# Kernel optimization log

Measured on AMD Instinct MI355X. Metric: run time of the kernel, lower is better.

## Reference

```python
import jax, jax.numpy as jnp
import numpy as np

NEG_SLOPE = 0.2
N, E, NNZ, IN, H, C = 100000, 50000, 800000, 128, 8, 16


def setup_inputs() -> dict:
    key = jax.random.key(0)
    ks = jax.random.split(key, 8)
    X = jax.random.normal(ks[0], (N, IN), jnp.float32)
    W_typed = jax.random.normal(ks[1], (4, IN, H * C), jnp.float32) * (1.0 / np.sqrt(IN))
    att_e = jax.random.normal(ks[2], (4, H, C), jnp.float32) * 0.1
    att_v = jax.random.normal(ks[3], (4, H, C), jnp.float32) * 0.1
    vertex = jax.random.randint(ks[4], (NNZ,), 0, N, jnp.int32)
    edges = jax.random.randint(ks[5], (NNZ,), 0, E, jnp.int32)
    vtype = jax.random.randint(ks[6], (N,), 0, 4, jnp.int32)
    etype = jax.random.randint(ks[7], (E,), 0, 4, jnp.int32)
    return {"X": X, "W_typed": W_typed, "att_e": att_e, "att_v": att_v,
            "vertex": vertex, "edges": edges, "vtype": vtype, "etype": etype}


def _segment_softmax(logits, seg, num):
    # numerically-stable softmax over segments (PyG-style, eps in denominator)
    m = jax.ops.segment_max(logits, seg, num_segments=num)
    ex = jnp.exp(logits - m[seg])
    s = jax.ops.segment_sum(ex, seg, num_segments=num)
    return ex / (s[seg] + 1e-16)


def reference(X, W_typed, att_e, att_v, vertex, edges, vtype, etype):
    # typed linear: project with all 4 type weights, select per node type
    Xall = jnp.einsum('ni,tio->tno', X, W_typed)        # [4, N, H*C]
    X0 = Xall[vtype, jnp.arange(N)]                     # [N, H*C]
    Xn = X0.reshape(N, H, C)
    Xve = Xn[vertex]                                    # [NNZ, H, C] gather vertex->incidence
    # vertex->edge attention, typed by edge type of each incidence
    beta = jnp.sum(Xve * att_e[etype[edges]], axis=-1)  # [NNZ, H]
    beta = jax.nn.leaky_relu(beta, NEG_SLOPE)
    beta = _segment_softmax(beta, edges, E)
    Xe = jax.nn.relu(jax.ops.segment_sum(Xve * beta[..., None], edges, num_segments=E))  # [E, H, C]
    Xe = Xe[edges]                                      # [NNZ, H, C] gather edge->incidence
    # edge->vertex attention, typed by node type of each incidence's vertex
    alpha = jnp.sum(Xe * att_v[vtype[vertex]], axis=-1)  # [NNZ, H]
    alpha = jax.nn.leaky_relu(alpha, NEG_SLOPE)
    alpha = _segment_softmax(alpha, vertex, N)
    Xv = jax.ops.segment_sum(Xe * alpha[..., None], vertex, num_segments=N)  # [N, H, C]
    return Xv.reshape(N, H * C)
```

## Files before the change

kernel.cpp:

```cpp
#include <hip/hip_runtime.h>

typedef __attribute__((ext_vector_type(8))) short bf16x8;
typedef __attribute__((ext_vector_type(4))) float f32x4;

#define NEG_SLOPE 0.2f

__device__ __forceinline__ unsigned short f2bf(float f){
  unsigned u = __float_as_uint(f);
  u = (u + 0x7fffu + ((u >> 16) & 1u)) >> 16;
  return (unsigned short)u;
}
__device__ __forceinline__ float bflo(unsigned u){ return __uint_as_float(u << 16); }
__device__ __forceinline__ float bfhi(unsigned u){ return __uint_as_float(u & 0xffff0000u); }
__device__ __forceinline__ float lrelu(float x){ return x > 0.f ? x : NEG_SLOPE * x; }

__global__ __launch_bounds__(256) void k_prep(
    const int* __restrict__ vtype, int N, int* __restrict__ tcnt, int nbHN,
    const float* __restrict__ W, short* __restrict__ Bfrag){
  __shared__ int lcnt[4];
  int b = (int)blockIdx.x;
  if (b < nbHN){
    if (threadIdx.x < 4) lcnt[threadIdx.x] = 0;
    __syncthreads();
    int i = b * 256 + threadIdx.x;
    if (i < N) atomicAdd(&lcnt[vtype[i]], 1);
    __syncthreads();
    if (threadIdx.x < 4 && lcnt[threadIdx.x] > 0)
      atomicAdd(tcnt + threadIdx.x, lcnt[threadIdx.x]);
    return;
  }
  b -= nbHN;
  int u = b * 256 + threadIdx.x;
  int j = u & 7, lane = (u >> 3) & 63, ct = (u >> 9) & 31, ks = u >> 14;
  int k = ks * 32 + ((lane >> 4) << 3) + j;
  int col = (ct << 4) + (lane & 15);
  int t = col >> 7, o = col & 127;
  Bfrag[u] = (short)f2bf(W[(t * 128 + k) * 128 + o]);
}

__global__ void k_pbase(const int* __restrict__ tcnt, int* __restrict__ pbase){
  if (threadIdx.x == 0 && blockIdx.x == 0){
    int pb = 0;
    for (int t = 0; t < 4; ++t){
      pbase[t] = pb;
      pb += ((tcnt[t] + 63) >> 6) << 6;
    }
    pbase[4] = pb;
  }
}

__global__ __launch_bounds__(256) void k_nodeplace(
    const int* __restrict__ vtype, int N, const int* __restrict__ pbase,
    int* __restrict__ tcur, int* __restrict__ nsorted){
  __shared__ int lcnt[4];
  __shared__ int gbase[4];
  int t = threadIdx.x;
  if (t < 4) lcnt[t] = 0;
  __syncthreads();
  int i = (int)blockIdx.x * 256 + t;
  int tt = 0, rank = 0;
  bool valid = i < N;
  if (valid){ tt = vtype[i]; rank = atomicAdd(&lcnt[tt], 1); }
  __syncthreads();
  if (t < 4 && lcnt[t] > 0) gbase[t] = atomicAdd(tcur + t, lcnt[t]);
  __syncthreads();
  if (valid) nsorted[pbase[tt] + gbase[tt] + rank] = i;
}

__global__ __launch_bounds__(256, 3) void k_gemm_hist(const float* __restrict__ X,
    const short* __restrict__ Bfrag, const int* __restrict__ nsorted,
    const int* __restrict__ pbase, unsigned short* __restrict__ X0,
    const int* __restrict__ edges, const int* __restrict__ vertex, int NNZ,
    int* __restrict__ cnt, int E,
    int* __restrict__ rank_e, int* __restrict__ rank_v, int nbHist){
  __shared__ short shB[8 * 4 * 64 * 8];
  const int tid = threadIdx.x;
  const int q = (int)blockIdx.x / 3, r = (int)blockIdx.x % 3;

  if (r != 0){
    int hb = 2 * q + (r - 1);
    if (hb < nbHist){
      int i = hb * 256 + tid;
      if (i < NNZ){
        rank_e[i] = atomicAdd(cnt + edges[i], 1);
        rank_v[i] = atomicAdd(cnt + E + vertex[i], 1);
      }
    }
    return;
  }

  const int rowIdx = q * 64;
  const int t = (rowIdx >= pbase[1]) + (rowIdx >= pbase[2]) + (rowIdx >= pbase[3]);

  const bf16x8* Bv = (const bf16x8*)Bfrag;
  bf16x8* shBv = (bf16x8*)shB;
  #pragma unroll
  for (int v = 0; v < 8; ++v){
    int item = v * 256 + tid;
    int slab = item >> 6, ln = item & 63;
    int ks = slab >> 3, ctl = slab & 7;
    shBv[item] = Bv[((ks * 32 + 8 * t + ctl) * 64) + ln];
  }

  const int w = tid >> 6, lane = tid & 63;
  const int m = lane & 15, qq = lane >> 4;
  const int node = nsorted[rowIdx + w * 16 + m];

  bf16x8 afrag[4];
  #pragma unroll
  for (int ks = 0; ks < 4; ++ks){
    bf16x8 f;
    if (node >= 0){
      const float4* src = (const float4*)(X + (size_t)node * 128 + ks * 32 + qq * 8);
      float4 a = src[0], b = src[1];
      f[0]=(short)f2bf(a.x); f[1]=(short)f2bf(a.y); f[2]=(short)f2bf(a.z); f[3]=(short)f2bf(a.w);
      f[4]=(short)f2bf(b.x); f[5]=(short)f2bf(b.y); f[6]=(short)f2bf(b.z); f[7]=(short)f2bf(b.w);
    } else {
      #pragma unroll
      for (int z = 0; z < 8; ++z) f[z] = 0;
    }
    afrag[ks] = f;
  }

  f32x4 acc[8];
  #pragma unroll
  for (int ct = 0; ct < 8; ++ct){
    acc[ct][0]=0.f; acc[ct][1]=0.f; acc[ct][2]=0.f; acc[ct][3]=0.f;
  }

  __syncthreads();
  #pragma unroll
  for (int ctl = 0; ctl < 8; ++ctl){
    #pragma unroll
    for (int ks = 0; ks < 4; ++ks){
      bf16x8 bf = shBv[(ks * 8 + ctl) * 64 + lane];
      acc[ctl] = __builtin_amdgcn_mfma_f32_16x16x32_bf16(afrag[ks], bf, acc[ctl], 0, 0, 0);
    }
  }

  const int col0 = lane & 15;
  #pragma unroll
  for (int rr = 0; rr < 4; ++rr){
    int row = nsorted[rowIdx + w * 16 + qq * 4 + rr];
    if (row < 0) continue;
    #pragma unroll
    for (int ctl = 0; ctl < 8; ++ctl)
      X0[(size_t)row * 128 + ctl * 16 + col0] = f2bf(acc[ctl][rr]);
  }
}

__global__ __launch_bounds__(256) void k_scanA(const int* __restrict__ cnt, int S,
                                               int* __restrict__ bsum){
  __shared__ int sh[256];
  int base = blockIdx.x * 1024 + threadIdx.x * 4;
  int s = 0;
  #pragma unroll
  for (int k = 0; k < 4; ++k){ int idx = base + k; if (idx < S) s += cnt[idx]; }
  sh[threadIdx.x] = s; __syncthreads();
  for (int off = 128; off > 0; off >>= 1){
    if (threadIdx.x < off) sh[threadIdx.x] += sh[threadIdx.x + off];
    __syncthreads();
  }
  if (threadIdx.x == 0) bsum[blockIdx.x] = sh[0];
}

__global__ void k_scanB2(int* bsum, int nb){
  if (threadIdx.x == 0 && blockIdx.x == 0){
    int run = 0;
    for (int b = 0; b < nb; ++b){ int v = bsum[b]; bsum[b] = run; run += v; }
  }
}

__global__ __launch_bounds__(256) void k_scanC2(const int* __restrict__ cnt, int S,
    const int* __restrict__ bsum, int* __restrict__ offs){
  __shared__ int sh[256];
  int t = threadIdx.x;
  int b = (int)blockIdx.x;
  int base = b * 1024 + t * 4;
  int c[4]; int s = 0;
  #pragma unroll
  for (int k = 0; k < 4; ++k){ int idx = base + k; c[k] = (idx < S) ? cnt[idx] : 0; s += c[k]; }
  sh[t] = s; __syncthreads();
  for (int off = 1; off < 256; off <<= 1){
    int v = (t >= off) ? sh[t - off] : 0; __syncthreads();
    sh[t] += v; __syncthreads();
  }
  int run = bsum[b] + sh[t] - s;
  #pragma unroll
  for (int k = 0; k < 4; ++k){
    int idx = base + k;
    if (idx < S){ offs[idx] = run; run += c[k]; }
  }
}

__global__ __launch_bounds__(256) void k_place(
    const int* __restrict__ edges, const int* __restrict__ vertex, int NNZ,
    const int* __restrict__ offs, const int* __restrict__ rank_e,
    const int* __restrict__ rank_v, int* __restrict__ rows, int E){
  int q = (int)blockIdx.x >> 1, r = (int)blockIdx.x & 1;
  int i = q * 256 + (int)threadIdx.x;
  if (i >= NNZ) return;
  if (r == 0) rows[offs[edges[i]]      + rank_e[i]] = vertex[i];
  else        rows[offs[E + vertex[i]] + rank_v[i]] = edges[i];
}

template<int OUT_BF16>
__device__ __forceinline__ void seg_body(const uint4* __restrict__ feat,
    const float* __restrict__ att, const int* __restrict__ rows_sorted,
    const int* __restrict__ offs, const int* __restrict__ cnt,
    const int* __restrict__ stype, void* __restrict__ outbuf,
    int S, int blockId, int tid){
  int wid = tid >> 6, lane = tid & 63;
  int s = blockId * 4 + wid;
  if (s >= S) return;
  int t = stype[s];
  int sub = lane >> 4, lane16 = lane & 15;
  const float4* ap = (const float4*)(att + t * 128 + lane16 * 8);
  float4 A0 = ap[0], A1 = ap[1];
  int start = offs[s], len = cnt[s];
  float denom = 0.f;
  float acc[8];
  #pragma unroll
  for (int e = 0; e < 8; ++e) acc[e] = 0.f;

  for (int base = 0; base < len; base += 64){
    int m = len - base; if (m > 64) m = 64;
    int idx = 0;
    if (lane < m) idx = rows_sorted[start + base + lane];
    int ng = (m + 3) >> 2;
    uint4 uA = make_uint4(0,0,0,0), uB = make_uint4(0,0,0,0);
    {
      int r0 = __shfl(idx, sub);
      if (sub < m) uA = feat[(size_t)r0 * 16 + lane16];
      int r1 = __shfl(idx, 4 + sub);
      if (4 + sub < m) uB = feat[(size_t)r1 * 16 + lane16];
    }
    for (int g = 0; g < ng; g += 2){
      {
        uint4 u = uA;
        int nr = (g + 2) * 4 + sub;
        int rn = __shfl(idx, nr & 63);
        if (nr < m) uA = feat[(size_t)rn * 16 + lane16];
        float x0 = bflo(u.x), x1 = bfhi(u.x), x2 = bflo(u.y), x3 = bfhi(u.y);
        float x4 = bflo(u.z), x5 = bfhi(u.z), x6 = bflo(u.w), x7 = bfhi(u.w);
        float p = x0*A0.x + x1*A0.y + x2*A0.z + x3*A0.w
                + x4*A1.x + x5*A1.y + x6*A1.z + x7*A1.w;
        p += __shfl_xor(p, 1);
        float wgt = __expf(lrelu(p));
        wgt = (g * 4 + sub < m) ? wgt : 0.f;
        denom += wgt;
        acc[0] += wgt*x0; acc[1] += wgt*x1; acc[2] += wgt*x2; acc[3] += wgt*x3;
        acc[4] += wgt*x4; acc[5] += wgt*x5; acc[6] += wgt*x6; acc[7] += wgt*x7;
      }
      if (g + 1 < ng){
        uint4 u = uB;
        int nr = (g + 3) * 4 + sub;
        int rn = __shfl(idx, nr & 63);
        if (nr < m) uB = feat[(size_t)rn * 16 + lane16];
        float x0 = bflo(u.x), x1 = bfhi(u.x), x2 = bflo(u.y), x3 = bfhi(u.y);
        float x4 = bflo(u.z), x5 = bfhi(u.z), x6 = bflo(u.w), x7 = bfhi(u.w);
        float p = x0*A0.x + x1*A0.y + x2*A0.z + x3*A0.w
                + x4*A1.x + x5*A1.y + x6*A1.z + x7*A1.w;
        p += __shfl_xor(p, 1);
        float wgt = __expf(lrelu(p));
        wgt = ((g + 1) * 4 + sub < m) ? wgt : 0.f;
        denom += wgt;
        acc[0] += wgt*x0; acc[1] += wgt*x1; acc[2] += wgt*x2; acc[3] += wgt*x3;
        acc[4] += wgt*x4; acc[5] += wgt*x5; acc[6] += wgt*x6; acc[7] += wgt*x7;
      }
    }
  }
  denom += __shfl_xor(denom, 16);
  denom += __shfl_xor(denom, 32);
  #pragma unroll
  for (int e = 0; e < 8; ++e){
    acc[e] += __shfl_xor(acc[e], 16);
    acc[e] += __shfl_xor(acc[e], 32);
  }
  float inv = 1.f / (denom + 1e-16f);
  float v[8];
  #pragma unroll
  for (int e = 0; e < 8; ++e) v[e] = acc[e] * inv;

  if constexpr (OUT_BF16){
    if (sub == 0){
      uint4 pw;
      pw.x = (unsigned)f2bf(fmaxf(v[0],0.f)) | ((unsigned)f2bf(fmaxf(v[1],0.f)) << 16);
      pw.y = (unsigned)f2bf(fmaxf(v[2],0.f)) | ((unsigned)f2bf(fmaxf(v[3],0.f)) << 16);
      pw.z = (unsigned)f2bf(fmaxf(v[4],0.f)) | ((unsigned)f2bf(fmaxf(v[5],0.f)) << 16);
      pw.w = (unsigned)f2bf(fmaxf(v[6],0.f)) | ((unsigned)f2bf(fmaxf(v[7],0.f)) << 16);
      ((uint4*)outbuf)[(size_t)s * 16 + lane16] = pw;
    }
  } else {
    if (sub == 0){
      float4* op = (float4*)outbuf;
      op[(size_t)s * 32 + lane16 * 2]     = make_float4(v[0], v[1], v[2], v[3]);
      op[(size_t)s * 32 + lane16 * 2 + 1] = make_float4(v[4], v[5], v[6], v[7]);
    }
  }
}

__global__ __launch_bounds__(256) void k_seg1(const uint4* __restrict__ X0,
    const float* __restrict__ att_e, const int* __restrict__ rows,
    const int* __restrict__ offs, const int* __restrict__ cnt,
    const int* __restrict__ etype, void* __restrict__ Xe, int E){
  seg_body<1>(X0, att_e, rows, offs, cnt, etype, Xe, E,
              (int)blockIdx.x, threadIdx.x);
}

__global__ __launch_bounds__(256) void k_seg2(const uint4* __restrict__ Xe,
    const float* __restrict__ att_v, const int* __restrict__ rows,
    const int* __restrict__ offs, const int* __restrict__ cnt,
    const int* __restrict__ vtype, float* __restrict__ out, int N){
  seg_body<0>(Xe, att_v, rows, offs, cnt, vtype, out, N,
              (int)blockIdx.x, threadIdx.x);
}

extern "C" void kernel_launch(void* const* d_in, const int* in_sizes, int n_in,
                              void* d_out, int out_size, void* d_ws, size_t ws_size,
                              hipStream_t stream){
  const float* X      = (const float*)d_in[0];
  const float* W      = (const float*)d_in[1];
  const float* att_e  = (const float*)d_in[2];
  const float* att_v  = (const float*)d_in[3];
  const int*   vertex = (const int*)d_in[4];
  const int*   edges  = (const int*)d_in[5];
  const int*   vtype  = (const int*)d_in[6];
  const int*   etype  = (const int*)d_in[7];
  float* out = (float*)d_out;
  const int N   = in_sizes[0] / 128;
  const int NNZ = in_sizes[4];
  const int E   = in_sizes[7];
  const int S   = E + N;

  const int nbI = (NNZ + 255) / 256;
  const int nbHN = (N + 255) / 256;
  const int nbS = (S + 1023) / 1024;
  const int nbSeg1 = (E + 3) / 4;
  const int nbPad = (N + 252 + 63) / 64;
  const int nsortedCap = nbPad * 64;

  char* wp = (char*)d_ws;
  int* cnt    = (int*)wp; wp += (size_t)S * 4;
  int* tcnt   = (int*)wp; wp += 16;
  int* tcur   = (int*)wp; wp += 16;
  int* offs   = (int*)wp; wp += (size_t)S * 4;
  int* bsum   = (int*)wp; wp += 1024;
  int* pbase  = (int*)wp; wp += 32;
  int* rows   = (int*)wp; wp += (size_t)2 * NNZ * 4;
  int* nsorted= (int*)wp; wp += (size_t)nsortedCap * 4;
  int* rank_e = (int*)wp; wp += (size_t)NNZ * 4;
  int* rank_v = (int*)wp; wp += (size_t)NNZ * 4;
  unsigned short* X0 = (unsigned short*)wp; wp += (size_t)N * 128 * 2;
  unsigned short* Xe = (unsigned short*)wp; wp += (size_t)E * 128 * 2;
  short* Bfrag = (short*)wp; wp += (size_t)65536 * 2;

  hipMemsetAsync(cnt, 0, (size_t)(S + 8) * 4, stream);
  hipMemsetAsync(nsorted, 0xFF, (size_t)nsortedCap * 4, stream);

  k_prep<<<nbHN + 256, 256, 0, stream>>>(vtype, N, tcnt, nbHN, W, Bfrag);
  k_pbase<<<1, 64, 0, stream>>>(tcnt, pbase);
  k_nodeplace<<<nbHN, 256, 0, stream>>>(vtype, N, pbase, tcur, nsorted);

  k_gemm_hist<<<3 * nbPad, 256, 0, stream>>>(X, Bfrag, nsorted, pbase,
      (unsigned short*)X0, edges, vertex, NNZ, cnt, E, rank_e, rank_v, nbI);

  k_scanA<<<nbS, 256, 0, stream>>>(cnt, S, bsum);
  k_scanB2<<<1, 64, 0, stream>>>(bsum, nbS);
  k_scanC2<<<nbS, 256, 0, stream>>>(cnt, S, bsum, offs);

  k_place<<<2 * nbI, 256, 0, stream>>>(edges, vertex, NNZ, offs,
      rank_e, rank_v, rows, E);

  k_seg1<<<nbSeg1, 256, 0, stream>>>((const uint4*)X0, att_e, rows,
      offs, cnt, etype, Xe, E);

  k_seg2<<<(N + 3) / 4, 256, 0, stream>>>((const uint4*)Xe, att_v,
      rows, offs + E, cnt + E, vtype, out, N);
}
```

Measured before the change: 316.6 us.

## Split CSR build into edge and vertex phases, overlap vertex histogram with seg1

New measurement: 320.0 us. Within noise of the previous version (+1.1%).

```diff
diff --git a/kernel.cpp b/kernel.cpp
--- a/kernel.cpp
+++ b/kernel.cpp
@@ -70,9 +70,8 @@
 __global__ __launch_bounds__(256, 3) void k_gemm_hist(const float* __restrict__ X,
     const short* __restrict__ Bfrag, const int* __restrict__ nsorted,
     const int* __restrict__ pbase, unsigned short* __restrict__ X0,
-    const int* __restrict__ edges, const int* __restrict__ vertex, int NNZ,
-    int* __restrict__ cnt, int E,
-    int* __restrict__ rank_e, int* __restrict__ rank_v, int nbHist){
+    const int* __restrict__ edges, int NNZ,
+    int* __restrict__ cnt, int* __restrict__ rank_e, int nbHist){
   __shared__ short shB[8 * 4 * 64 * 8];
   const int tid = threadIdx.x;
   const int q = (int)blockIdx.x / 3, r = (int)blockIdx.x % 3;
@@ -81,10 +80,7 @@
     int hb = 2 * q + (r - 1);
     if (hb < nbHist){
       int i = hb * 256 + tid;
-      if (i < NNZ){
-        rank_e[i] = atomicAdd(cnt + edges[i], 1);
-        rank_v[i] = atomicAdd(cnt + E + vertex[i], 1);
-      }
+      if (i < NNZ) rank_e[i] = atomicAdd(cnt + edges[i], 1);
     }
     return;
   }
@@ -193,15 +189,20 @@
   }
 }
 
-__global__ __launch_bounds__(256) void k_place(
+__global__ __launch_bounds__(256) void k_place_e(
     const int* __restrict__ edges, const int* __restrict__ vertex, int NNZ,
     const int* __restrict__ offs, const int* __restrict__ rank_e,
-    const int* __restrict__ rank_v, int* __restrict__ rows, int E){
-  int q = (int)blockIdx.x >> 1, r = (int)blockIdx.x & 1;
-  int i = q * 256 + (int)threadIdx.x;
-  if (i >= NNZ) return;
-  if (r == 0) rows[offs[edges[i]]      + rank_e[i]] = vertex[i];
-  else        rows[offs[E + vertex[i]] + rank_v[i]] = edges[i];
+    int* __restrict__ rows){
+  int i = (int)blockIdx.x * 256 + (int)threadIdx.x;
+  if (i < NNZ) rows[offs[edges[i]] + rank_e[i]] = vertex[i];
+}
+
+__global__ __launch_bounds__(256) void k_place_v(
+    const int* __restrict__ edges, const int* __restrict__ vertex, int NNZ,
+    const int* __restrict__ offsV, const int* __restrict__ rank_v,
+    int* __restrict__ rowsV){
+  int i = (int)blockIdx.x * 256 + (int)threadIdx.x;
+  if (i < NNZ) rowsV[offsV[vertex[i]] + rank_v[i]] = edges[i];
 }
 
 template<int OUT_BF16>
@@ -300,12 +301,24 @@
   }
 }
 
-__global__ __launch_bounds__(256) void k_seg1(const uint4* __restrict__ X0,
-    const float* __restrict__ att_e, const int* __restrict__ rows,
-    const int* __restrict__ offs, const int* __restrict__ cnt,
-    const int* __restrict__ etype, void* __restrict__ Xe, int E){
-  seg_body<1>(X0, att_e, rows, offs, cnt, etype, Xe, E,
-              (int)blockIdx.x, threadIdx.x);
+__global__ __launch_bounds__(256) void k_seg1_histv(
+    const int* __restrict__ vertex, int NNZ,
+    int* __restrict__ cntV, int* __restrict__ rank_v, int nbHist,
+    const uint4* __restrict__ X0, const float* __restrict__ att_e,
+    const int* __restrict__ rows, const int* __restrict__ offs,
+    const int* __restrict__ cnt, const int* __restrict__ etype,
+    void* __restrict__ Xe, int E, int nbSeg){
+  const int q = (int)blockIdx.x / 5, r = (int)blockIdx.x % 5;
+  if (r == 0){
+    if (q < nbHist){
+      int i = q * 256 + (int)threadIdx.x;
+      if (i < NNZ) rank_v[i] = atomicAdd(cntV + vertex[i], 1);
+    }
+    return;
+  }
+  int segBlk = q * 4 + (r - 1);
+  if (segBlk >= nbSeg) return;
+  seg_body<1>(X0, att_e, rows, offs, cnt, etype, Xe, E, segBlk, threadIdx.x);
 }
 
 __global__ __launch_bounds__(256) void k_seg2(const uint4* __restrict__ Xe,
@@ -335,10 +348,13 @@
 
   const int nbI = (NNZ + 255) / 256;
   const int nbHN = (N + 255) / 256;
-  const int nbS = (S + 1023) / 1024;
+  const int nbSE = (E + 1023) / 1024;
+  const int nbSV = (N + 1023) / 1024;
   const int nbSeg1 = (E + 3) / 4;
   const int nbPad = (N + 252 + 63) / 64;
   const int nsortedCap = nbPad * 64;
+  const int nQA = (nbPad > (nbI + 1) / 2) ? nbPad : (nbI + 1) / 2;
+  const int nQB = (nbI > (nbSeg1 + 3) / 4) ? nbI : (nbSeg1 + 3) / 4;
 
   char* wp = (char*)d_ws;
   int* cnt    = (int*)wp; wp += (size_t)S * 4;
@@ -362,19 +378,23 @@
   k_pbase<<<1, 64, 0, stream>>>(tcnt, pbase);
   k_nodeplace<<<nbHN, 256, 0, stream>>>(vtype, N, pbase, tcur, nsorted);
 
-  k_gemm_hist<<<3 * nbPad, 256, 0, stream>>>(X, Bfrag, nsorted, pbase,
-      (unsigned short*)X0, edges, vertex, NNZ, cnt, E, rank_e, rank_v, nbI);
-
-  k_scanA<<<nbS, 256, 0, stream>>>(cnt, S, bsum);
-  k_scanB2<<<1, 64, 0, stream>>>(bsum, nbS);
-  k_scanC2<<<nbS, 256, 0, stream>>>(cnt, S, bsum, offs);
-
-  k_place<<<2 * nbI, 256, 0, stream>>>(edges, vertex, NNZ, offs,
-      rank_e, rank_v, rows, E);
-
-  k_seg1<<<nbSeg1, 256, 0, stream>>>((const uint4*)X0, att_e, rows,
-      offs, cnt, etype, Xe, E);
+  k_gemm_hist<<<3 * nQA, 256, 0, stream>>>(X, Bfrag, nsorted, pbase,
+      (unsigned short*)X0, edges, NNZ, cnt, rank_e, nbI);
+
+  k_scanA<<<nbSE, 256, 0, stream>>>(cnt, E, bsum);
+  k_scanB2<<<1, 64, 0, stream>>>(bsum, nbSE);
+  k_scanC2<<<nbSE, 256, 0, stream>>>(cnt, E, bsum, offs);
+  k_place_e<<<nbI, 256, 0, stream>>>(edges, vertex, NNZ, offs, rank_e, rows);
+
+  k_seg1_histv<<<5 * nQB, 256, 0, stream>>>(vertex, NNZ, cnt + E, rank_v, nbI,
+      (const uint4*)X0, att_e, rows, offs, cnt, etype, Xe, E, nbSeg1);
+
+  k_scanA<<<nbSV, 256, 0, stream>>>(cnt + E, N, bsum);
+  k_scanB2<<<1, 64, 0, stream>>>(bsum, nbSV);
+  k_scanC2<<<nbSV, 256, 0, stream>>>(cnt + E, N, bsum, offs + E);
+  k_place_v<<<nbI, 256, 0, stream>>>(edges, vertex, NNZ, offs + E, rank_v,
+      rows + NNZ);
 
   k_seg2<<<(N + 3) / 4, 256, 0, stream>>>((const uint4*)Xe, att_v,
-      rows, offs + E, cnt + E, vtype, out, N);
-}
+      rows + NNZ, offs + E, cnt + E, vtype, out, N);
+}
```
